# Performance work log

Measured on AMD Instinct MI355X. Metric: run time of the kernel, lower is better.

Reference implementation:

```python
import jax, jax.numpy as jnp
import numpy as np
from jax import lax

SCORE_THRESH = 0.05
NMS_THRESH = 0.5
DET_PER_IMG = 100
WX, WY, WW, WH = 10.0, 10.0, 5.0, 5.0   # BoxCoder weights
BBOX_XFORM_CLIP = float(np.log(1000.0 / 16.0))
NEG = -1e9  # sentinel for invalid / suppressed scores


def setup_inputs() -> dict:
    key = jax.random.key(0)
    k1, k2, k3 = jax.random.split(key, 3)
    R, C = 1000, 81
    W, H = 1333, 800
    class_logits = jax.random.normal(k1, (R, C), dtype=jnp.float32)
    box_regression = jax.random.normal(k2, (R, C * 4), dtype=jnp.float32)
    # build valid xyxy proposal boxes inside the image from uniform noise
    u = jax.random.uniform(k3, (R, 4), dtype=jnp.float32)
    x1 = u[:, 0] * (W - 120)
    y1 = u[:, 1] * (H - 120)
    x2 = jnp.minimum(x1 + 20.0 + u[:, 2] * 300.0, W - 1)
    y2 = jnp.minimum(y1 + 20.0 + u[:, 3] * 300.0, H - 1)
    proposals = jnp.stack([x1, y1, x2, y2], axis=1)
    return {"class_logits": class_logits, "box_regression": box_regression,
            "proposals": proposals, "image_w": W, "image_h": H}


def _decode(rel, boxes):
    """BoxCoder.decode: rel [R, C*4], boxes [R,4] xyxy -> [R, C, 4]."""
    w = boxes[:, 2] - boxes[:, 0] + 1.0
    h = boxes[:, 3] - boxes[:, 1] + 1.0
    cx = boxes[:, 0] + 0.5 * w
    cy = boxes[:, 1] + 0.5 * h
    dx = rel[:, 0::4] / WX
    dy = rel[:, 1::4] / WY
    dw = jnp.minimum(rel[:, 2::4] / WW, BBOX_XFORM_CLIP)
    dh = jnp.minimum(rel[:, 3::4] / WH, BBOX_XFORM_CLIP)
    pcx = dx * w[:, None] + cx[:, None]
    pcy = dy * h[:, None] + cy[:, None]
    pw = jnp.exp(dw) * w[:, None]
    ph = jnp.exp(dh) * h[:, None]
    return jnp.stack([pcx - 0.5 * pw, pcy - 0.5 * ph,
                      pcx + 0.5 * pw - 1.0, pcy + 0.5 * ph - 1.0], axis=-1)


def _pairwise_iou(b):
    """Legacy (+1) IoU: b [N,4] -> [N,N]."""
    area = (b[:, 2] - b[:, 0] + 1.0) * (b[:, 3] - b[:, 1] + 1.0)
    lt = jnp.maximum(b[:, None, :2], b[None, :, :2])
    rb = jnp.minimum(b[:, None, 2:], b[None, :, 2:])
    wh = jnp.clip(rb - lt + 1.0, 0.0)
    inter = wh[..., 0] * wh[..., 1]
    return inter / (area[:, None] + area[None, :] - inter)


def _nms_one_class(boxes, scores):
    """Greedy NMS for one class, fixed shape. Returns keep mask [N] in original order."""
    N = scores.shape[0]
    valid = scores > SCORE_THRESH
    order = jnp.argsort(-jnp.where(valid, scores, NEG))
    b = boxes[order]
    v = valid[order]
    iou = _pairwise_iou(b)  # [N,N], descending-score order
    idx = jnp.arange(N)

    def body(keep, xs):
        i, row, vi = xs
        suppressed = jnp.any(keep & (row > NMS_THRESH) & (idx < i))
        keep = keep.at[i].set(vi & jnp.logical_not(suppressed))
        return keep, None

    keep_sorted, _ = lax.scan(body, jnp.zeros(N, bool), (idx, iou, v))
    return jnp.zeros(N, bool).at[order].set(keep_sorted)


def _forward(class_logits, box_regression, proposals, image_w, image_h):
    probs = jax.nn.softmax(class_logits, axis=-1)          # [R, C]
    boxes = _decode(box_regression, proposals)             # [R, C, 4]
    # clip_to_image (remove_empty=False), legacy -1 convention
    x = jnp.clip(boxes[..., 0::2], 0.0, image_w - 1)
    y = jnp.clip(boxes[..., 1::2], 0.0, image_h - 1)
    boxes = jnp.stack([x[..., 0], y[..., 0], x[..., 1], y[..., 1]], axis=-1)
    # drop background class 0
    sc = probs[:, 1:].T                                    # [C-1, R]
    bc = jnp.transpose(boxes[:, 1:, :], (1, 0, 2))         # [C-1, R, 4]
    keep = jax.vmap(_nms_one_class)(bc, sc)                # [C-1, R]
    flat_s = jnp.where(keep, sc, NEG).reshape(-1)
    top_s, top_i = lax.top_k(flat_s, DET_PER_IMG)
    top_b = bc.reshape(-1, 4)[top_i]
    labels = top_i // sc.shape[1] + 1
    return top_s, top_b, labels


def reference(class_logits, box_regression, proposals, image_w, image_h):
    return _forward(class_logits, box_regression, proposals, image_w, image_h)
```

## Files before the change

kernel.cpp:

```cpp
#include <hip/hip_runtime.h>
#include <cmath>

#define R_ROWS 1000
#define NCLS   81
#define REGW   (NCLS * 4)
#define SCORE_T 0.05f
#define NMS_T   0.5f
#define NEG_S  -1e9f
#define DETS   100
#define CLIP_V 4.135166556742356f
#define MAXC   1000

#define NBINS   1024
#define SEL_CAP 2048
#define CAP_DEFAULT 20000


__device__ __forceinline__ float4 decode_clip(const float* __restrict__ prop,
                                              const float* __restrict__ reg,
                                              int r, int ccol, float wmax, float hmax) {
    float x1 = prop[r * 4 + 0], y1 = prop[r * 4 + 1];
    float x2 = prop[r * 4 + 2], y2 = prop[r * 4 + 3];
    float w  = __fadd_rn(__fsub_rn(x2, x1), 1.0f);
    float h  = __fadd_rn(__fsub_rn(y2, y1), 1.0f);
    float cx = __fadd_rn(x1, __fmul_rn(0.5f, w));
    float cy = __fadd_rn(y1, __fmul_rn(0.5f, h));
    const float* rr = reg + r * REGW + 4 * ccol;
    float dx = rr[0] / 10.0f;
    float dy = rr[1] / 10.0f;
    float dw = fminf(rr[2] / 5.0f, CLIP_V);
    float dh = fminf(rr[3] / 5.0f, CLIP_V);
    float pcx = __fadd_rn(__fmul_rn(dx, w), cx);
    float pcy = __fadd_rn(__fmul_rn(dy, h), cy);
    float pw  = __fmul_rn(expf(dw), w);
    float ph  = __fmul_rn(expf(dh), h);
    float ox1 = __fsub_rn(pcx, __fmul_rn(0.5f, pw));
    float oy1 = __fsub_rn(pcy, __fmul_rn(0.5f, ph));
    float ox2 = __fsub_rn(__fadd_rn(pcx, __fmul_rn(0.5f, pw)), 1.0f);
    float oy2 = __fsub_rn(__fadd_rn(pcy, __fmul_rn(0.5f, ph)), 1.0f);
    float4 o;
    o.x = fminf(fmaxf(ox1, 0.0f), wmax);
    o.y = fminf(fmaxf(oy1, 0.0f), hmax);
    o.z = fminf(fmaxf(ox2, 0.0f), wmax);
    o.w = fminf(fmaxf(oy2, 0.0f), hmax);
    return o;
}

__device__ __forceinline__ float iou_legacy(float ax1, float ay1, float ax2, float ay2,
                                            float bx1, float by1, float bx2, float by2) {
    float aw = __fadd_rn(__fsub_rn(ax2, ax1), 1.0f);
    float ah = __fadd_rn(__fsub_rn(ay2, ay1), 1.0f);
    float areaA = __fmul_rn(aw, ah);
    float bw = __fadd_rn(__fsub_rn(bx2, bx1), 1.0f);
    float bh = __fadd_rn(__fsub_rn(by2, by1), 1.0f);
    float areaB = __fmul_rn(bw, bh);
    float ltx = fmaxf(ax1, bx1), lty = fmaxf(ay1, by1);
    float rbx = fminf(ax2, bx2), rby = fminf(ay2, by2);
    float wx = fmaxf(__fadd_rn(__fsub_rn(rbx, ltx), 1.0f), 0.0f);
    float wy = fmaxf(__fadd_rn(__fsub_rn(rby, lty), 1.0f), 0.0f);
    float inter = __fmul_rn(wx, wy);
    float denom = __fsub_rn(__fadd_rn(areaA, areaB), inter);
    return inter / denom;
}

__device__ __forceinline__ int bin_of(float s) {
    int idx = (int)(__float_as_uint(s) >> 16) - 0x3D00;
    return idx < 0 ? 0 : (idx > NBINS - 1 ? NBINS - 1 : idx);
}

__device__ __forceinline__ unsigned long long key_of(float s, unsigned f) {
    return ((unsigned long long)__float_as_uint(s) << 32) | (unsigned long long)(~f);
}


__global__ __launch_bounds__(64) void k_softmax_stats(const float* __restrict__ logits,
                                                      float* __restrict__ rowmax,
                                                      float* __restrict__ rowsum,
                                                      int* __restrict__ gcount,
                                                      int* __restrict__ hist) {
    int r = blockIdx.x;
    int l = threadIdx.x;
    if (r < NBINS / 64) hist[r * 64 + l] = 0;
    if (r == 0 && l == 0) *gcount = 0;
    float v1 = logits[r * NCLS + l];
    float v2 = (l < NCLS - 64) ? logits[r * NCLS + 64 + l] : -INFINITY;
    float m = fmaxf(v1, v2);
    #pragma unroll
    for (int off = 32; off; off >>= 1) m = fmaxf(m, __shfl_xor(m, off));
    float s = expf(__fsub_rn(v1, m));
    if (l < NCLS - 64) s = __fadd_rn(s, expf(__fsub_rn(v2, m)));
    #pragma unroll
    for (int off = 32; off; off >>= 1) s = __fadd_rn(s, __shfl_xor(s, off));
    if (l == 0) { rowmax[r] = m; rowsum[r] = s; }
}


__global__ __launch_bounds__(64) void k_nms_class(const float* __restrict__ logits,
                                                  const float* __restrict__ reg,
                                                  const float* __restrict__ prop,
                                                  const float* __restrict__ rowmax,
                                                  const float* __restrict__ rowsum,
                                                  const int* __restrict__ piw,
                                                  const int* __restrict__ pih,
                                                  float* __restrict__ kscores,
                                                  int* __restrict__ kflats,
                                                  int* __restrict__ gcount,
                                                  int* __restrict__ hist,
                                                  int cap) {
    __shared__ float us[MAXC];    __shared__ int uidx[MAXC];
    __shared__ float ss[MAXC];    __shared__ int sidx[MAXC];
    __shared__ float bx[MAXC][4];
    __shared__ int   supp[MAXC];
    __shared__ int   cnt;

    const int cidx = blockIdx.x;
    const int ccol = cidx + 1;
    const int t = threadIdx.x;

    if (t == 0) cnt = 0;
    __syncthreads();

    for (int r = t; r < R_ROWS; r += 64) {
        float z = logits[r * NCLS + ccol];
        float s = expf(__fsub_rn(z, rowmax[r])) / rowsum[r];
        if (s > SCORE_T) {
            int p = atomicAdd(&cnt, 1);
            us[p] = s; uidx[p] = r;
        }
    }
    __syncthreads();
    const int M = cnt;

    for (int i = t; i < M; i += 64) {
        float si = us[i]; int ri = uidx[i];
        int rank = 0;
        for (int j = 0; j < M; j++) {
            float sj = us[j]; int rj = uidx[j];
            rank += (sj > si) || (sj == si && rj < ri);
        }
        ss[rank] = si; sidx[rank] = ri;
    }
    __syncthreads();

    const float wmax = (float)(*piw - 1);
    const float hmax = (float)(*pih - 1);
    for (int i = t; i < M; i += 64) {
        float4 b = decode_clip(prop, reg, sidx[i], ccol, wmax, hmax);
        bx[i][0] = b.x; bx[i][1] = b.y; bx[i][2] = b.z; bx[i][3] = b.w;
        supp[i] = 0;
    }
    __syncthreads();

    for (int i = 0; i < M; i++) {
        if (!supp[i]) {
            float ax1 = bx[i][0], ay1 = bx[i][1], ax2 = bx[i][2], ay2 = bx[i][3];
            for (int j = i + 1 + t; j < M; j += 64) {
                if (!supp[j]) {
                    float v = iou_legacy(ax1, ay1, ax2, ay2,
                                         bx[j][0], bx[j][1], bx[j][2], bx[j][3]);
                    if (v > NMS_T) supp[j] = 1;
                }
            }
        }
        __syncthreads();
    }

    for (int i = t; i < M; i += 64) {
        if (!supp[i]) {
            int p = atomicAdd(gcount, 1);
            if (p < cap) {
                kscores[p] = ss[i];
                kflats[p]  = cidx * R_ROWS + sidx[i];
                atomicAdd(&hist[bin_of(ss[i])], 1);
            }
        }
    }
}


__global__ __launch_bounds__(256) void k_select(const float* __restrict__ kscores,
                                                const int* __restrict__ kflats,
                                                const int* __restrict__ gcount,
                                                int cap,
                                                const int* __restrict__ hist,
                                                const float* __restrict__ reg,
                                                const float* __restrict__ prop,
                                                const int* __restrict__ piw,
                                                const int* __restrict__ pih,
                                                float* __restrict__ out) {
    __shared__ int cs[256];
    __shared__ unsigned long long ck[SEL_CAP + 4];
    __shared__ float sel_s[DETS]; __shared__ int sel_f[DETS];
    __shared__ int sh_cut, sh_mcnt;

    const int t = threadIdx.x;
    int K = *gcount; if (K > cap) K = cap;
    const int target = (K < DETS) ? K : DETS;

    int v0 = hist[4 * t], v1 = hist[4 * t + 1], v2 = hist[4 * t + 2], v3 = hist[4 * t + 3];
    int s3 = v3, s2 = v2 + s3, s1 = v1 + s2, s0 = v0 + s1;
    cs[t] = s0;
    __syncthreads();
    for (int off = 1; off < 256; off <<= 1) {
        int x = cs[t] + ((t + off < 256) ? cs[t + off] : 0);
        __syncthreads();
        cs[t] = x;
        __syncthreads();
    }
    int tail = (t < 255) ? cs[t + 1] : 0;
    int S0 = s0 + tail, S1 = s1 + tail, S2 = s2 + tail, S3 = s3 + tail;
    if (t == 0) { sh_cut = 0; sh_mcnt = 0; }
    __syncthreads();
    if (target > 0) {
        int best = -1;
        if      (S3 >= target) best = 4 * t + 3;
        else if (S2 >= target) best = 4 * t + 2;
        else if (S1 >= target) best = 4 * t + 1;
        else if (S0 >= target) best = 4 * t;
        if (best >= 0) atomicMax(&sh_cut, best);
    }
    __syncthreads();
    const int cut = sh_cut;

    for (int i = t; i < K; i += 256) {
        float s = kscores[i];
        if (bin_of(s) >= cut) {
            int p = atomicAdd(&sh_mcnt, 1);
            if (p < SEL_CAP) ck[p] = key_of(s, (unsigned)kflats[i]);
        }
    }
    __syncthreads();
    const int Mc = sh_mcnt;

    if (Mc <= SEL_CAP) {
        int Mp = (Mc + 3) & ~3;
        if (t < Mp - Mc) ck[Mc + t] = 0;
        __syncthreads();
        for (int i = t; i < Mc; i += 256) {
            unsigned long long ki = ck[i];
            int r = 0;
            for (int j = 0; j < Mp; j += 4)
                r += (int)(ck[j] > ki) + (int)(ck[j + 1] > ki)
                   + (int)(ck[j + 2] > ki) + (int)(ck[j + 3] > ki);
            if (r < DETS) {
                sel_s[r] = __uint_as_float((unsigned)(ki >> 32));
                sel_f[r] = (int)(~(unsigned)ki);
            }
        }
    } else {
        for (int i = t; i < K; i += 256) {
            float s = kscores[i];
            if (bin_of(s) < cut) continue;
            unsigned long long ki = key_of(s, (unsigned)kflats[i]);
            int r = 0;
            for (int j = 0; j < K; j++)
                r += (int)(key_of(kscores[j], (unsigned)kflats[j]) > ki);
            if (r < DETS) {
                sel_s[r] = __uint_as_float((unsigned)(ki >> 32));
                sel_f[r] = (int)(~(unsigned)ki);
            }
        }
    }
    __syncthreads();

    if (t == 0 && target < DETS) {
        int n = target, f = 0;
        while (n < DETS) {
            bool used = false;
            for (int q = 0; q < K; q++) if (kflats[q] == f) { used = true; break; }
            if (!used) { sel_s[n] = NEG_S; sel_f[n] = f; n++; }
            f++;
        }
    }
    __syncthreads();

    const float wmax = (float)(*piw - 1);
    const float hmax = (float)(*pih - 1);
    if (t < DETS) {
        int f = sel_f[t];
        int cidx = f / R_ROWS;
        int r    = f % R_ROWS;
        float4 b = decode_clip(prop, reg, r, cidx + 1, wmax, hmax);
        out[t] = sel_s[t];
        out[DETS + 4 * t + 0] = b.x;
        out[DETS + 4 * t + 1] = b.y;
        out[DETS + 4 * t + 2] = b.z;
        out[DETS + 4 * t + 3] = b.w;
        out[DETS * 5 + t] = (float)(cidx + 1);
    }
}


extern "C" void kernel_launch(void* const* d_in, const int* in_sizes, int n_in,
                              void* d_out, int out_size, void* d_ws, size_t ws_size,
                              hipStream_t stream) {
    (void)in_sizes; (void)n_in; (void)out_size;
    const float* logits = (const float*)d_in[0];
    const float* reg    = (const float*)d_in[1];
    const float* prop   = (const float*)d_in[2];
    const int*   piw    = (const int*)d_in[3];
    const int*   pih    = (const int*)d_in[4];
    float* out = (float*)d_out;

    char* ws = (char*)d_ws;
    int*   hist    = (int*)(ws);
    int*   gcount  = (int*)(ws + 4096);
    float* rowmax  = (float*)(ws + 4224);
    float* rowsum  = (float*)(ws + 8256);
    char*  listbuf = ws + 12288;

    long avail = (long)ws_size - 12288;
    int cap = CAP_DEFAULT;
    if (avail < (long)cap * 8) cap = (int)(avail / 8);
    if (cap < 1) cap = 1;
    float* kscores = (float*)listbuf;
    int*   kflats  = (int*)(listbuf + (size_t)cap * 4);

    k_softmax_stats<<<dim3(R_ROWS), dim3(64), 0, stream>>>(logits, rowmax, rowsum, gcount, hist);
    k_nms_class<<<dim3(NCLS - 1), dim3(64), 0, stream>>>(logits, reg, prop, rowmax, rowsum,
                                                         piw, pih, kscores, kflats, gcount, hist, cap);
    k_select<<<dim3(1), dim3(256), 0, stream>>>(kscores, kflats, gcount, cap, hist,
                                                reg, prop, piw, pih, out);
}
```

Baseline: 44.81 us.

## Fuse top-k select into NMS kernel via last-block completion counter

Merges the single-block selection kernel into the per-class NMS kernel. A global done counter lets the last finishing block run the histogram-based top-k and output decode, which removes one kernel launch. Each NMS block also grows from 64 to 256 threads, so the ranking, decode and suppression loops run with more parallel lanes. The costs are extra shared memory per block, threadfence overhead, and a larger per-iteration __syncthreads cost in the serial NMS loop.

```diff
diff --git a/kernel.cpp b/kernel.cpp
--- a/kernel.cpp
+++ b/kernel.cpp
@@ -14,6 +14,7 @@
 #define NBINS   1024
 #define SEL_CAP 2048
 #define CAP_DEFAULT 20000
+#define NBLK_CLS (NCLS - 1)
 
 
 __device__ __forceinline__ float4 decode_clip(const float* __restrict__ prop,
@@ -77,11 +78,12 @@
                                                       float* __restrict__ rowmax,
                                                       float* __restrict__ rowsum,
                                                       int* __restrict__ gcount,
+                                                      int* __restrict__ done,
                                                       int* __restrict__ hist) {
     int r = blockIdx.x;
     int l = threadIdx.x;
     if (r < NBINS / 64) hist[r * 64 + l] = 0;
-    if (r == 0 && l == 0) *gcount = 0;
+    if (r == 0 && l == 0) { *gcount = 0; *done = 0; }
     float v1 = logits[r * NCLS + l];
     float v2 = (l < NCLS - 64) ? logits[r * NCLS + 64 + l] : -INFINITY;
     float m = fmaxf(v1, v2);
@@ -95,32 +97,41 @@
 }
 
 
-__global__ __launch_bounds__(64) void k_nms_class(const float* __restrict__ logits,
-                                                  const float* __restrict__ reg,
-                                                  const float* __restrict__ prop,
-                                                  const float* __restrict__ rowmax,
-                                                  const float* __restrict__ rowsum,
-                                                  const int* __restrict__ piw,
-                                                  const int* __restrict__ pih,
-                                                  float* __restrict__ kscores,
-                                                  int* __restrict__ kflats,
-                                                  int* __restrict__ gcount,
-                                                  int* __restrict__ hist,
-                                                  int cap) {
+__global__ __launch_bounds__(256) void k_nms_select(const float* __restrict__ logits,
+                                                    const float* __restrict__ reg,
+                                                    const float* __restrict__ prop,
+                                                    const float* __restrict__ rowmax,
+                                                    const float* __restrict__ rowsum,
+                                                    const int* __restrict__ piw,
+                                                    const int* __restrict__ pih,
+                                                    float* __restrict__ kscores,
+                                                    int* __restrict__ kflats,
+                                                    int* __restrict__ gcount,
+                                                    int* __restrict__ done,
+                                                    int* __restrict__ hist,
+                                                    int cap,
+                                                    float* __restrict__ out) {
     __shared__ float us[MAXC];    __shared__ int uidx[MAXC];
     __shared__ float ss[MAXC];    __shared__ int sidx[MAXC];
     __shared__ float bx[MAXC][4];
     __shared__ int   supp[MAXC];
     __shared__ int   cnt;
+    __shared__ int   sh_last;
+    __shared__ int cs[256];
+    __shared__ unsigned long long ck[SEL_CAP + 4];
+    __shared__ float sel_s[DETS]; __shared__ int sel_f[DETS];
+    __shared__ int sh_cut, sh_mcnt;
 
     const int cidx = blockIdx.x;
     const int ccol = cidx + 1;
     const int t = threadIdx.x;
+    const float wmax = (float)(*piw - 1);
+    const float hmax = (float)(*pih - 1);
 
     if (t == 0) cnt = 0;
     __syncthreads();
 
-    for (int r = t; r < R_ROWS; r += 64) {
+    for (int r = t; r < R_ROWS; r += 256) {
         float z = logits[r * NCLS + ccol];
         float s = expf(__fsub_rn(z, rowmax[r])) / rowsum[r];
         if (s > SCORE_T) {
@@ -131,7 +142,7 @@
     __syncthreads();
     const int M = cnt;
 
-    for (int i = t; i < M; i += 64) {
+    for (int i = t; i < M; i += 256) {
         float si = us[i]; int ri = uidx[i];
         int rank = 0;
         for (int j = 0; j < M; j++) {
@@ -142,9 +153,7 @@
     }
     __syncthreads();
 
-    const float wmax = (float)(*piw - 1);
-    const float hmax = (float)(*pih - 1);
-    for (int i = t; i < M; i += 64) {
+    for (int i = t; i < M; i += 256) {
         float4 b = decode_clip(prop, reg, sidx[i], ccol, wmax, hmax);
         bx[i][0] = b.x; bx[i][1] = b.y; bx[i][2] = b.z; bx[i][3] = b.w;
         supp[i] = 0;
@@ -154,7 +163,7 @@
     for (int i = 0; i < M; i++) {
         if (!supp[i]) {
             float ax1 = bx[i][0], ay1 = bx[i][1], ax2 = bx[i][2], ay2 = bx[i][3];
-            for (int j = i + 1 + t; j < M; j += 64) {
+            for (int j = i + 1 + t; j < M; j += 256) {
                 if (!supp[j]) {
                     float v = iou_legacy(ax1, ay1, ax2, ay2,
                                          bx[j][0], bx[j][1], bx[j][2], bx[j][3]);
@@ -165,7 +174,7 @@
         __syncthreads();
     }
 
-    for (int i = t; i < M; i += 64) {
+    for (int i = t; i < M; i += 256) {
         if (!supp[i]) {
             int p = atomicAdd(gcount, 1);
             if (p < cap) {
@@ -175,25 +184,14 @@
             }
         }
     }
-}
-
-
-__global__ __launch_bounds__(256) void k_select(const float* __restrict__ kscores,
-                                                const int* __restrict__ kflats,
-                                                const int* __restrict__ gcount,
-                                                int cap,
-                                                const int* __restrict__ hist,
-                                                const float* __restrict__ reg,
-                                                const float* __restrict__ prop,
-                                                const int* __restrict__ piw,
-                                                const int* __restrict__ pih,
-                                                float* __restrict__ out) {
-    __shared__ int cs[256];
-    __shared__ unsigned long long ck[SEL_CAP + 4];
-    __shared__ float sel_s[DETS]; __shared__ int sel_f[DETS];
-    __shared__ int sh_cut, sh_mcnt;
-
-    const int t = threadIdx.x;
+
+    __threadfence();
+    __syncthreads();
+    if (t == 0) sh_last = (atomicAdd(done, 1) == NBLK_CLS - 1) ? 1 : 0;
+    __syncthreads();
+    if (!sh_last) return;
+    __threadfence();
+
     int K = *gcount; if (K > cap) K = cap;
     const int target = (K < DETS) ? K : DETS;
 
@@ -274,19 +272,17 @@
     }
     __syncthreads();
 
-    const float wmax = (float)(*piw - 1);
-    const float hmax = (float)(*pih - 1);
     if (t < DETS) {
         int f = sel_f[t];
-        int cidx = f / R_ROWS;
-        int r    = f % R_ROWS;
-        float4 b = decode_clip(prop, reg, r, cidx + 1, wmax, hmax);
+        int c2 = f / R_ROWS;
+        int r  = f % R_ROWS;
+        float4 b = decode_clip(prop, reg, r, c2 + 1, wmax, hmax);
         out[t] = sel_s[t];
         out[DETS + 4 * t + 0] = b.x;
         out[DETS + 4 * t + 1] = b.y;
         out[DETS + 4 * t + 2] = b.z;
         out[DETS + 4 * t + 3] = b.w;
-        out[DETS * 5 + t] = (float)(cidx + 1);
+        out[DETS * 5 + t] = (float)(c2 + 1);
     }
 }
 
@@ -305,6 +301,7 @@
     char* ws = (char*)d_ws;
     int*   hist    = (int*)(ws);
     int*   gcount  = (int*)(ws + 4096);
+    int*   done    = (int*)(ws + 4160);
     float* rowmax  = (float*)(ws + 4224);
     float* rowsum  = (float*)(ws + 8256);
     char*  listbuf = ws + 12288;
@@ -316,9 +313,9 @@
     float* kscores = (float*)listbuf;
     int*   kflats  = (int*)(listbuf + (size_t)cap * 4);
 
-    k_softmax_stats<<<dim3(R_ROWS), dim3(64), 0, stream>>>(logits, rowmax, rowsum, gcount, hist);
-    k_nms_class<<<dim3(NCLS - 1), dim3(64), 0, stream>>>(logits, reg, prop, rowmax, rowsum,
-                                                         piw, pih, kscores, kflats, gcount, hist, cap);
-    k_select<<<dim3(1), dim3(256), 0, stream>>>(kscores, kflats, gcount, cap, hist,
-                                                reg, prop, piw, pih, out);
-}
+    k_softmax_stats<<<dim3(R_ROWS), dim3(64), 0, stream>>>(logits, rowmax, rowsum,
+                                                           gcount, done, hist);
+    k_nms_select<<<dim3(NBLK_CLS), dim3(256), 0, stream>>>(logits, reg, prop, rowmax, rowsum,
+                                                           piw, pih, kscores, kflats,
+                                                           gcount, done, hist, cap, out);
+}
```

New measurement: 41.76 us. 1.07x faster.
